# Optimization experiments

Measured on AMD Instinct MI355X. Metric: run time of the kernel, lower is better.

Reference implementation:

```python
import jax, jax.numpy as jnp
import numpy as np

N_NODES = 100000
N_EDGES = 1600000
N_FEAT = 48
N_EDGE_FEAT = 16
HIDDEN = 128


def setup_inputs() -> dict:
    key = jax.random.key(0)
    ks = jax.random.split(key, 8)
    tot = 2 * N_FEAT + N_EDGE_FEAT  # 112
    s1 = 1.0 / np.sqrt(tot)
    s2 = 1.0 / np.sqrt(HIDDEN)
    return {
        "x": jax.random.normal(ks[0], (N_NODES, N_FEAT), dtype=jnp.float32),
        "edge_index": jax.random.randint(ks[1], (2, N_EDGES), 0, N_NODES, dtype=jnp.int64),
        "edge_feat": jax.random.normal(ks[2], (N_EDGES, N_EDGE_FEAT), dtype=jnp.float32),
        "W1": jax.random.normal(ks[3], (tot, HIDDEN), dtype=jnp.float32) * s1,
        "b1": jnp.zeros((HIDDEN,), dtype=jnp.float32),
        "W2": jax.random.normal(ks[4], (HIDDEN, HIDDEN), dtype=jnp.float32) * s2,
        "b2": jnp.zeros((HIDDEN,), dtype=jnp.float32),
        "W3": jax.random.normal(ks[5], (HIDDEN, N_FEAT), dtype=jnp.float32) * s2,
        "b3": jnp.zeros((N_FEAT,), dtype=jnp.float32),
    }


def reference(x, edge_index, edge_feat, W1, b1, W2, b2, W3, b3):
    source = edge_index[0]
    target = edge_index[1]
    # gather + concat: (n_edges, 2*n_feat + n_edge_feat)
    edge = jnp.concatenate([x[source], x[target], edge_feat], axis=-1)
    # 3-layer MLP with ReLU
    h = jax.nn.relu(edge @ W1 + b1)
    h = jax.nn.relu(h @ W2 + b2)
    message = h @ W3 + b3  # (n_edges, n_feat)
    # scatter-mean over target indices
    n = x.shape[0]
    msum = jax.ops.segment_sum(message, target, num_segments=n)
    cnt = jax.ops.segment_sum(jnp.ones((target.shape[0],), dtype=x.dtype), target, num_segments=n)
    update = msum / jnp.maximum(cnt, 1.0)[:, None]  # empty segments -> 0
    return x + update
```

## Files before the change

### kernel.cpp

```cpp
#include <hip/hip_runtime.h>
#include <hip/hip_bf16.h>


#define NN 100000
#define NE 1600000
#define NF 48
#define TOT 112
#define HID 128
#define TILE 256
#define NTILE 6250

typedef __attribute__((ext_vector_type(8))) short short8;
typedef __attribute__((ext_vector_type(4))) float floatx4;

__device__ __forceinline__ unsigned short f2bf(float f) {
    union { float f; unsigned u; } v; v.f = f;
    unsigned u = v.u;
    return (unsigned short)((u + 0x7FFFu + ((u >> 16) & 1u)) >> 16);
}
__device__ __forceinline__ unsigned pk2(float a, float b) {
    __hip_bfloat162 h = __float22bfloat162_rn(make_float2(a, b));
    return *(unsigned*)&h;
}

__device__ __forceinline__ void bar_lgkm() {
    asm volatile("s_waitcnt lgkmcnt(0)" ::: "memory");
    __builtin_amdgcn_s_barrier();
}

__global__ void hist_prep_kernel(const int* __restrict__ ei, int* __restrict__ cnt,
                                 const float* __restrict__ W1, const float* __restrict__ W2,
                                 const float* __restrict__ W3,
                                 unsigned short* __restrict__ wt1,
                                 unsigned short* __restrict__ wt2,
                                 unsigned short* __restrict__ wt3) {
    if (blockIdx.x < NTILE) {
        int e = blockIdx.x * 256 + threadIdx.x;
        atomicAdd(cnt + ei[NE + e], 1);
        return;
    }
    int idx = (blockIdx.x - NTILE) * 256 + threadIdx.x;
    if (idx < 16384) {
        int n = idx >> 7, k = idx & 127;
        wt1[idx] = (k < TOT) ? f2bf(W1[k * HID + n]) : (unsigned short)0;
    } else if (idx < 32768) {
        int j = idx - 16384; int n = j >> 7, k = j & 127;
        wt2[j] = f2bf(W2[k * HID + n]);
    } else if (idx < 38912) {
        int j = idx - 32768; int n = j >> 7, k = j & 127;
        wt3[j] = f2bf(W3[k * NF + n]);
    }
}

__global__ void scan_kernel(const int* __restrict__ cnt, int* __restrict__ off,
                            int* __restrict__ counter) {
    __shared__ int sd[256];
    __shared__ int sbase;
    int tid = threadIdx.x;
    int n = blockIdx.x * 256 + tid;
    int v = (n < NN) ? cnt[n] : 0;
    sd[tid] = v;
    __syncthreads();
#pragma unroll
    for (int d = 1; d < 256; d <<= 1) {
        int t = (tid >= d) ? sd[tid - d] : 0;
        __syncthreads();
        sd[tid] += t;
        __syncthreads();
    }
    if (tid == 255) sbase = atomicAdd(counter, sd[255]);
    __syncthreads();
    if (n < NN) off[n] = sbase + sd[tid] - v;
}

__global__ void place_kernel(const int* __restrict__ ei, int* __restrict__ off,
                             unsigned long long* __restrict__ srt) {
    int e = blockIdx.x * 256 + threadIdx.x;
    int t = ei[NE + e];
    int p = atomicAdd(off + t, 1);
    srt[p] = (unsigned long long)e | ((unsigned long long)ei[e] << 21) |
             ((unsigned long long)t << 38);
}

__device__ __forceinline__ const short8* frag_ptr(const unsigned short* base, int row, int s,
                                                  int lane15, int quad) {
    return (const short8*)((const char*)base + row * 256 + (((s * 4 + quad) ^ lane15) << 4));
}

__device__ __forceinline__ void gather_issue(const float* __restrict__ x,
                                             const float* __restrict__ ef,
                                             unsigned long long pk, int sub, float4* v) {
    int eid = (int)(pk & 0x1FFFFFull);
    int src = (int)((pk >> 21) & 0x1FFFFull);
    int tgt = (int)(pk >> 38);
#pragma unroll
    for (int j = 0; j < 14; ++j) {
        int p = 2 * j + sub;
        const float4* gp;
        if (p < 12)      gp = (const float4*)(x + 48 * (size_t)src) + p;
        else if (p < 24) gp = (const float4*)(x + 48 * (size_t)tgt) + (p - 12);
        else             gp = (const float4*)(ef + 16 * (size_t)eid) + (p - 24);
        v[j] = *gp;
    }
}

__launch_bounds__(512, 2)
__global__ void gemm_kernel(const float* __restrict__ x, const float* __restrict__ ef,
                            const unsigned long long* __restrict__ srt,
                            const unsigned short* __restrict__ wt1,
                            const unsigned short* __restrict__ wt2,
                            const unsigned short* __restrict__ wt3,
                            const float* __restrict__ b1, const float* __restrict__ b2,
                            float* __restrict__ out_acc) {
    __shared__ __align__(16) unsigned short lw1[128 * 128];
    __shared__ __align__(16) unsigned short lw2[128 * 128];
    __shared__ __align__(16) unsigned short lw3[48 * 128];
    __shared__ __align__(16) unsigned short ea[TILE * 128];
    __shared__ float lb1[128], lb2[128];
    __shared__ int ltgt[TILE];
    __shared__ int seg_start[TILE + 4];
    __shared__ int seg_tgt[TILE];
    __shared__ int nseg;

    const int tid = threadIdx.x;
    const uint4* s1 = (const uint4*)wt1;
    for (int i = tid; i < 2048; i += 512) {
        int n = i >> 4, g = i & 15;
        *(uint4*)((char*)lw1 + n * 256 + ((g ^ (n & 15)) << 4)) = s1[i];
    }
    const uint4* s2 = (const uint4*)wt2;
    for (int i = tid; i < 2048; i += 512) {
        int n = i >> 4, g = i & 15;
        *(uint4*)((char*)lw2 + n * 256 + ((g ^ (n & 15)) << 4)) = s2[i];
    }
    const uint4* s3 = (const uint4*)wt3;
    for (int i = tid; i < 768; i += 512) {
        int n = i >> 4, g = i & 15;
        *(uint4*)((char*)lw3 + n * 256 + ((g ^ (n & 15)) << 4)) = s3[i];
    }
    if (tid < 128) lb1[tid] = b1[tid];
    else if (tid < 256) lb2[tid - 128] = b2[tid - 128];
    __syncthreads();

    const int l15 = tid & 15;
    const int q = (tid & 63) >> 4;
    const int ln = tid & 63;
    const int wave = tid >> 6;
    const int sub = ln & 1;
    const int grow = wave * 32 + (ln >> 1);
    const int gl15 = grow & 15;
    const int G = gridDim.x;

    unsigned long long pkCur = srt[(size_t)blockIdx.x * TILE + grow];
    unsigned long long pkNext = (blockIdx.x + G < NTILE)
        ? srt[(size_t)(blockIdx.x + G) * TILE + grow] : 0ull;
    float4 v[14];
    gather_issue(x, ef, pkCur, sub, v);

    for (int tile = blockIdx.x; tile < NTILE; tile += G) {
        {
            int tgt = (int)(pkCur >> 38);
            if (sub == 0) ltgt[grow] = tgt;
#pragma unroll
            for (int j = 0; j < 14; ++j) {
                uint2 h = make_uint2(pk2(v[j].x, v[j].y), pk2(v[j].z, v[j].w));
                *(uint2*)((char*)ea + grow * 256 + ((j ^ gl15) << 4) + (sub << 3)) = h;
            }
            *(uint4*)((char*)ea + grow * 256 + (((14 + sub) ^ gl15) << 4)) =
                make_uint4(0u, 0u, 0u, 0u);
        }
        {
            unsigned long long pkN2 = 0ull;
            if (tile + 2 * G < NTILE)
                pkN2 = srt[(size_t)(tile + 2 * G) * TILE + grow];
            if (tile + G < NTILE)
                gather_issue(x, ef, pkNext, sub, v);
            pkCur = pkNext;
            pkNext = pkN2;
        }
        __builtin_amdgcn_sched_barrier(0);

        __builtin_amdgcn_s_setprio(1);
#pragma unroll
        for (int layer = 0; layer < 2; ++layer) {
            const unsigned short* lw = layer ? lw2 : lw1;
            const float* lb = layer ? lb2 : lb1;
            short8 bf[2][4];
#pragma unroll
            for (int gi = 0; gi < 2; ++gi)
#pragma unroll
                for (int s = 0; s < 4; ++s)
                    bf[gi][s] = *frag_ptr(ea, (wave * 2 + gi) * 16 + l15, s, l15, q);
#pragma unroll
            for (int mt = 0; mt < 8; ++mt) {
                floatx4 a0 = (floatx4){0.f, 0.f, 0.f, 0.f};
                floatx4 a1 = (floatx4){0.f, 0.f, 0.f, 0.f};
#pragma unroll
                for (int s = 0; s < 4; ++s) {
                    short8 a = *frag_ptr(lw, mt * 16 + l15, s, l15, q);
                    a0 = __builtin_amdgcn_mfma_f32_16x16x32_bf16(a, bf[0][s], a0, 0, 0, 0);
                    a1 = __builtin_amdgcn_mfma_f32_16x16x32_bf16(a, bf[1][s], a1, 0, 0, 0);
                }
                int f0 = mt * 16 + q * 4;
                const float4 bv = *(const float4*)(lb + f0);
                uint2 h0 = make_uint2(pk2(fmaxf(a0[0] + bv.x, 0.f), fmaxf(a0[1] + bv.y, 0.f)),
                                      pk2(fmaxf(a0[2] + bv.z, 0.f), fmaxf(a0[3] + bv.w, 0.f)));
                uint2 h1 = make_uint2(pk2(fmaxf(a1[0] + bv.x, 0.f), fmaxf(a1[1] + bv.y, 0.f)),
                                      pk2(fmaxf(a1[2] + bv.z, 0.f), fmaxf(a1[3] + bv.w, 0.f)));
                int gran = 2 * mt + (q >> 1), off8 = (q & 1) << 3;
                *(uint2*)((char*)ea + (wave * 32 + l15) * 256 + ((gran ^ l15) << 4) + off8) = h0;
                *(uint2*)((char*)ea + (wave * 32 + 16 + l15) * 256 + ((gran ^ l15) << 4) + off8) = h1;
            }
        }
        {
            short8 bf[2][4];
#pragma unroll
            for (int gi = 0; gi < 2; ++gi)
#pragma unroll
                for (int s = 0; s < 4; ++s)
                    bf[gi][s] = *frag_ptr(ea, (wave * 2 + gi) * 16 + l15, s, l15, q);
#pragma unroll
            for (int mt = 0; mt < 3; ++mt) {
                floatx4 a0 = (floatx4){0.f, 0.f, 0.f, 0.f};
                floatx4 a1 = (floatx4){0.f, 0.f, 0.f, 0.f};
#pragma unroll
                for (int s = 0; s < 4; ++s) {
                    short8 a = *frag_ptr(lw3, mt * 16 + l15, s, l15, q);
                    a0 = __builtin_amdgcn_mfma_f32_16x16x32_bf16(a, bf[0][s], a0, 0, 0, 0);
                    a1 = __builtin_amdgcn_mfma_f32_16x16x32_bf16(a, bf[1][s], a1, 0, 0, 0);
                }
                int gran = mt * 4 + q;
                *(float4*)((char*)ea + (wave * 32 + l15) * 256 + ((gran ^ l15) << 4)) =
                    *(float4*)&a0;
                *(float4*)((char*)ea + (wave * 32 + 16 + l15) * 256 + ((gran ^ l15) << 4)) =
                    *(float4*)&a1;
            }
        }
        __builtin_amdgcn_s_setprio(0);
        bar_lgkm();
        if (wave == 0) {
            int base = 0;
#pragma unroll
            for (int c = 0; c < 4; ++c) {
                int p = c * 64 + ln;
                int t = ltgt[p];
                int flag = (p == 0) || (t != ltgt[p - 1]);
                unsigned long long mask = __ballot(flag);
                int sid = base + __popcll(mask & ((1ull << ln) - 1ull));
                if (flag) { seg_start[sid] = p; seg_tgt[sid] = t; }
                base += __popcll(mask);
            }
            if (ln == 0) { nseg = base; seg_start[base] = TILE; }
        }
        bar_lgkm();
        if (ln < 48) {
            const int gcol = ln >> 2, coff = (ln & 3) << 2;
            const int ns = nseg;
            for (int s = wave; s < ns; s += 8) {
                int a = seg_start[s], bnd = seg_start[s + 1];
                float s0 = 0.f, s1f = 0.f;
                int p = a;
                for (; p + 1 < bnd; p += 2) {
                    s0  += *(const float*)((const char*)ea + p * 256 +
                                           ((gcol ^ (p & 15)) << 4) + coff);
                    s1f += *(const float*)((const char*)ea + (p + 1) * 256 +
                                           ((gcol ^ ((p + 1) & 15)) << 4) + coff);
                }
                if (p < bnd)
                    s0 += *(const float*)((const char*)ea + p * 256 +
                                          ((gcol ^ (p & 15)) << 4) + coff);
                float sum = s0 + s1f;
                float* dst = out_acc + 48 * (size_t)seg_tgt[s] + ln;
                if (s == 0 || s == ns - 1) atomicAdd(dst, sum);
                else *dst = sum;
            }
        }
        bar_lgkm();
    }
}

__global__ void finalize_kernel(const float* __restrict__ x, const int* __restrict__ cnt,
                                const float* __restrict__ b3, float* __restrict__ out) {
    int i = blockIdx.x * 256 + threadIdx.x;
    if (i >= NN * 12) return;
    int node = i / 12, j = i % 12;
    float c = (float)cnt[node];
    float4 xv = ((const float4*)x)[i];
    float4 ov = ((const float4*)out)[i];
    float4 bv = ((const float4*)b3)[j];
    float4 r;
    if (c > 0.f) {
        float rc = 1.f / c;
        r.x = xv.x + ov.x * rc + bv.x;
        r.y = xv.y + ov.y * rc + bv.y;
        r.z = xv.z + ov.z * rc + bv.z;
        r.w = xv.w + ov.w * rc + bv.w;
    } else {
        r = xv;
    }
    ((float4*)out)[i] = r;
}

extern "C" void kernel_launch(void* const* d_in, const int* in_sizes, int n_in,
                              void* d_out, int out_size, void* d_ws, size_t ws_size,
                              hipStream_t stream) {
    const float* x  = (const float*)d_in[0];
    const int*   ei = (const int*)d_in[1];
    const float* ef = (const float*)d_in[2];
    const float* W1 = (const float*)d_in[3];
    const float* b1 = (const float*)d_in[4];
    const float* W2 = (const float*)d_in[5];
    const float* b2 = (const float*)d_in[6];
    const float* W3 = (const float*)d_in[7];
    const float* b3 = (const float*)d_in[8];
    float* out = (float*)d_out;

    char* ws = (char*)d_ws;
    int* cnt     = (int*)ws;
    int* counter = (int*)(ws + 400000);
    int* off     = (int*)(ws + 409600);
    unsigned short* wt1 = (unsigned short*)(ws + 819456);
    unsigned short* wt2 = wt1 + 16384;
    unsigned short* wt3 = wt2 + 16384;
    unsigned long long* srt = (unsigned long long*)(ws + 901120);

    hipMemsetAsync(out, 0, (size_t)out_size * sizeof(float), stream);
    hipMemsetAsync(cnt, 0, (size_t)NN * sizeof(int) + 4, stream);
    hist_prep_kernel<<<NTILE + 152, 256, 0, stream>>>(ei, cnt, W1, W2, W3, wt1, wt2, wt3);
    scan_kernel<<<391, 256, 0, stream>>>(cnt, off, counter);
    place_kernel<<<6250, 256, 0, stream>>>(ei, off, srt);
    gemm_kernel<<<256, 512, 0, stream>>>(x, ef, srt, wt1, wt2, wt3, b1, b2, out);
    finalize_kernel<<<4688, 256, 0, stream>>>(x, cnt, b3, out);
}
```

Measured before the change: 560.1 us.

## Make segment reduction wave-local to drop block-wide barriers per tile

Each wave now finds the target-run boundaries of its own 32 sorted edges with shuffle and ballot while staging the gather. It then reduces those runs straight from its own rows of the shared tile. This removes the block-wide segment scan by wave 0 and the three barriers per tile, so waves can proceed independently between tiles. In exchange, runs that cross wave boundaries are split, which adds atomic adds to the output accumulator. It also relies on each wave only ever touching its own rows of the shared edge buffer.

```diff
diff --git a/kernel.cpp b/kernel.cpp
--- a/kernel.cpp
+++ b/kernel.cpp
@@ -21,11 +21,6 @@
 __device__ __forceinline__ unsigned pk2(float a, float b) {
     __hip_bfloat162 h = __float22bfloat162_rn(make_float2(a, b));
     return *(unsigned*)&h;
-}
-
-__device__ __forceinline__ void bar_lgkm() {
-    asm volatile("s_waitcnt lgkmcnt(0)" ::: "memory");
-    __builtin_amdgcn_s_barrier();
 }
 
 __global__ void hist_prep_kernel(const int* __restrict__ ei, int* __restrict__ cnt,
@@ -117,10 +112,8 @@
     __shared__ __align__(16) unsigned short lw3[48 * 128];
     __shared__ __align__(16) unsigned short ea[TILE * 128];
     __shared__ float lb1[128], lb2[128];
-    __shared__ int ltgt[TILE];
-    __shared__ int seg_start[TILE + 4];
-    __shared__ int seg_tgt[TILE];
-    __shared__ int nseg;
+    __shared__ int wseg_start[8][33];
+    __shared__ int wseg_tgt[8][32];
 
     const int tid = threadIdx.x;
     const uint4* s1 = (const uint4*)wt1;
@@ -158,9 +151,20 @@
     gather_issue(x, ef, pkCur, sub, v);
 
     for (int tile = blockIdx.x; tile < NTILE; tile += G) {
+        int nrun;
         {
             int tgt = (int)(pkCur >> 38);
-            if (sub == 0) ltgt[grow] = tgt;
+            int tprev = __shfl(tgt, ln - 2);
+            int r = ln >> 1;
+            int startf = (r == 0) || (tgt != tprev);
+            unsigned long long mask = __ballot(startf && (sub == 0));
+            nrun = __popcll(mask);
+            if (startf && sub == 0) {
+                int sid = __popcll(mask & ((1ull << ln) - 1ull));
+                wseg_start[wave][sid] = r;
+                wseg_tgt[wave][sid] = tgt;
+            }
+            if (ln == 0) wseg_start[wave][nrun] = 32;
 #pragma unroll
             for (int j = 0; j < 14; ++j) {
                 uint2 h = make_uint2(pk2(v[j].x, v[j].y), pk2(v[j].z, v[j].w));
@@ -237,45 +241,26 @@
             }
         }
         __builtin_amdgcn_s_setprio(0);
-        bar_lgkm();
-        if (wave == 0) {
-            int base = 0;
-#pragma unroll
-            for (int c = 0; c < 4; ++c) {
-                int p = c * 64 + ln;
-                int t = ltgt[p];
-                int flag = (p == 0) || (t != ltgt[p - 1]);
-                unsigned long long mask = __ballot(flag);
-                int sid = base + __popcll(mask & ((1ull << ln) - 1ull));
-                if (flag) { seg_start[sid] = p; seg_tgt[sid] = t; }
-                base += __popcll(mask);
-            }
-            if (ln == 0) { nseg = base; seg_start[base] = TILE; }
-        }
-        bar_lgkm();
         if (ln < 48) {
             const int gcol = ln >> 2, coff = (ln & 3) << 2;
-            const int ns = nseg;
-            for (int s = wave; s < ns; s += 8) {
-                int a = seg_start[s], bnd = seg_start[s + 1];
+            const char* wbase = (const char*)ea + wave * 32 * 256;
+            for (int k = 0; k < nrun; ++k) {
+                int a = wseg_start[wave][k], bnd = wseg_start[wave][k + 1];
                 float s0 = 0.f, s1f = 0.f;
                 int p = a;
                 for (; p + 1 < bnd; p += 2) {
-                    s0  += *(const float*)((const char*)ea + p * 256 +
-                                           ((gcol ^ (p & 15)) << 4) + coff);
-                    s1f += *(const float*)((const char*)ea + (p + 1) * 256 +
+                    s0  += *(const float*)(wbase + p * 256 + ((gcol ^ (p & 15)) << 4) + coff);
+                    s1f += *(const float*)(wbase + (p + 1) * 256 +
                                            ((gcol ^ ((p + 1) & 15)) << 4) + coff);
                 }
                 if (p < bnd)
-                    s0 += *(const float*)((const char*)ea + p * 256 +
-                                          ((gcol ^ (p & 15)) << 4) + coff);
+                    s0 += *(const float*)(wbase + p * 256 + ((gcol ^ (p & 15)) << 4) + coff);
                 float sum = s0 + s1f;
-                float* dst = out_acc + 48 * (size_t)seg_tgt[s] + ln;
-                if (s == 0 || s == ns - 1) atomicAdd(dst, sum);
+                float* dst = out_acc + 48 * (size_t)wseg_tgt[wave][k] + ln;
+                if (k == 0 || k == nrun - 1) atomicAdd(dst, sum);
                 else *dst = sum;
             }
         }
-        bar_lgkm();
     }
 }
 
```

Result: faster. 521.7 us (-6.9%).
